# Performance work log

Hardware: AMD Instinct MI355X
Metric: run time of the kernel (lower is better)

The kernel has to match this reference:

```python
import jax, jax.numpy as jnp
import numpy as np

BATCH = 4096
NUM_CLASSES = 10000
FEAT_DIM = 512


def setup_inputs() -> dict:
    key = jax.random.key(0)
    k1, k2, k3 = jax.random.split(key, 3)
    x = jax.random.normal(k1, (BATCH, FEAT_DIM), dtype=jnp.float32)
    labels = jax.random.randint(k2, (BATCH,), 0, NUM_CLASSES)
    centers = jax.random.normal(k3, (NUM_CLASSES, FEAT_DIM), dtype=jnp.float32)
    lr = jnp.array([0.1], dtype=jnp.float32)
    return {"x": x, "labels": labels, "centers": centers, "lr": lr}


def reference(x, labels, centers, lr):
    batch, feat_dim = x.shape
    n_classes = centers.shape[0]

    # --- center update (vectorized replacement of the per-class/per-sample double loop) ---
    # A_j = count_j * centers[j] - sum_{i: label_i==j} x_i ;  delta_j = A_j / (1 + count_j)
    ones = jnp.ones((batch,), dtype=x.dtype)
    counts = jax.ops.segment_sum(ones, labels, num_segments=n_classes)          # [C]
    sum_x = jax.ops.segment_sum(x, labels, num_segments=n_classes)              # [C, D]
    delta = (counts[:, None] * centers - sum_x) / (1.0 + counts[:, None])       # [C, D]
    # torch wraps the result in a fresh nn.Parameter -> detached from autograd graph
    centers_new = jax.lax.stop_gradient(centers - lr[0] * delta)

    # --- pairwise squared distances, then 1/(1+d) ---
    d = (jnp.sum(x * x, axis=1, keepdims=True)                                   # [B, 1]
         + jnp.sum(centers_new * centers_new, axis=1)[None, :]                   # [1, C]
         - 2.0 * (x @ centers_new.T))                                            # [B, C]
    d = 1.0 / (1.0 + d)

    # --- masked reduction: row sum minus the own-class entry, clamped ---
    row_sum = d.sum(axis=1)                                                      # [B]
    own = jnp.take_along_axis(d, labels[:, None], axis=1)[:, 0]                  # [B]
    dist = jnp.clip(row_sum - own, 1e-12, 1e12)
    return dist.mean()
```

## Files before the change

kernel.cpp:

```cpp
#include <hip/hip_runtime.h>
#include <hip/hip_bf16.h>

#define BATCH 4096
#define NCLS  10000
#define CPAD  10240
#define FDIM  512
#define MAXL  32

typedef float f32x4 __attribute__((ext_vector_type(4)));
typedef int   ix4   __attribute__((ext_vector_type(4)));
typedef int   ix8   __attribute__((ext_vector_type(8)));

__device__ static inline void gld_lds16(const void* g, void* l) {
    __builtin_amdgcn_global_load_lds(
        (const __attribute__((address_space(1))) void*)g,
        (__attribute__((address_space(3))) void*)l, 16, 0, 0);
}

__device__ static inline unsigned int fp4e(float v) {
    unsigned int s = (__float_as_uint(v) >> 31) << 3;
    float a = fabsf(v);
    unsigned int c;
    if      (a < 1.25f) c = (a < 0.75f) ? (a < 0.25f ? 0u : 1u) : 2u;
    else if (a < 2.5f)  c = (a < 1.75f) ? 3u : 4u;
    else                c = (a < 3.5f) ? 5u : (a < 5.f ? 6u : 7u);
    return s | c;
}

__device__ static inline int pdst4(int row, int k) {
    return (row >> 4) * 4096 + (k >> 7) * 1024
         + ((k >> 5) & 3) * 256 + (row & 15) * 16 + ((k & 31) >> 1);
}

__global__ void prep_all(const float* __restrict__ x, const int* __restrict__ labels,
                         const float* __restrict__ centers, const float* __restrict__ lr,
                         unsigned char* __restrict__ xq, float* __restrict__ xnorm,
                         unsigned char* __restrict__ cq, float* __restrict__ cnorm,
                         float* __restrict__ out) {
    const int bid = blockIdx.x, t = threadIdx.x;
    __shared__ float red[4];
    if (bid < BATCH) {
        if (bid == 0 && t == 0) out[0] = 0.f;
        int i = bid;
        float2 v = *(const float2*)&x[(size_t)i * FDIM + 2 * t];
        xq[pdst4(i, 2 * t)] = (unsigned char)(fp4e(v.x) | (fp4e(v.y) << 4));
        float s = v.x * v.x + v.y * v.y;
#pragma unroll
        for (int m = 1; m < 64; m <<= 1) s += __shfl_xor(s, m);
        if ((t & 63) == 0) red[t >> 6] = s;
        __syncthreads();
        if (t == 0) xnorm[i] = red[0] + red[1] + red[2] + red[3];
        return;
    }
    int j = bid - BATCH;
    if (j >= NCLS) {
        cq[pdst4(j, 2 * t)] = 0;
        if (t == 0) cnorm[j] = 1e30f;
        return;
    }
    __shared__ int nmatch;
    __shared__ int idxs[MAXL];
    if (t == 0) nmatch = 0;
    __syncthreads();
    {
        const int4* l4 = (const int4*)labels;
        int4 a0 = l4[t], a1 = l4[t + 256], a2 = l4[t + 512], a3 = l4[t + 768];
#define CHK(V, B) { \
        if (V.x == j) { int p = atomicAdd(&nmatch, 1); if (p < MAXL) idxs[p] = (B); } \
        if (V.y == j) { int p = atomicAdd(&nmatch, 1); if (p < MAXL) idxs[p] = (B) + 1; } \
        if (V.z == j) { int p = atomicAdd(&nmatch, 1); if (p < MAXL) idxs[p] = (B) + 2; } \
        if (V.w == j) { int p = atomicAdd(&nmatch, 1); if (p < MAXL) idxs[p] = (B) + 3; } }
        CHK(a0, 4 * t) CHK(a1, 4 * (t + 256)) CHK(a2, 4 * (t + 512)) CHK(a3, 4 * (t + 768))
#undef CHK
    }
    __syncthreads();
    int cfull = nmatch;
    int c = cfull > MAXL ? MAXL : cfull;
    if (t == 0 && c > 1) {
        for (int a = 1; a < c; ++a) {
            int v = idxs[a]; int b = a - 1;
            while (b >= 0 && idxs[b] > v) { idxs[b + 1] = idxs[b]; --b; }
            idxs[b + 1] = v;
        }
    }
    __syncthreads();
    float cf  = (float)cfull;
    float lr0 = lr[0];
    float inv = 1.f / (1.f + cf);
    float c0 = centers[(size_t)j * FDIM + 2 * t];
    float c1 = centers[(size_t)j * FDIM + 2 * t + 1];
    float sx0 = 0.f, sx1 = 0.f;
    for (int q = 0; q < c; ++q) {
        const float* xr = &x[(size_t)idxs[q] * FDIM + 2 * t];
        sx0 += xr[0]; sx1 += xr[1];
    }
    float n0 = c0 - lr0 * (cf * c0 - sx0) * inv;
    float n1 = c1 - lr0 * (cf * c1 - sx1) * inv;
    cq[pdst4(j, 2 * t)] = (unsigned char)(fp4e(n0) | (fp4e(n1) << 4));
    float cn2 = n0 * n0 + n1 * n1;
#pragma unroll
    for (int m = 1; m < 64; m <<= 1) cn2 += __shfl_xor(cn2, m);
    if ((t & 63) == 0) red[t >> 6] = cn2;
    __syncthreads();
    if (t == 0) cnorm[j] = red[0] + red[1] + red[2] + red[3];
}

__global__ void __launch_bounds__(256, 2)
pairwise(const unsigned char* __restrict__ xq, const unsigned char* __restrict__ cq,
         const float* __restrict__ xnorm, const float* __restrict__ cnorm,
         const int* __restrict__ labels, float* __restrict__ row_part) {
    __shared__ unsigned char Als[32768];
    __shared__ unsigned char Bls[2][16384];
    __shared__ unsigned char Cnls[4096];
    const int tid = threadIdx.x;
    const int w = tid >> 6, lane = tid & 63;
    const int lr16 = lane & 15, lhi = lane >> 4;
    const int bid = blockIdx.x;
    const int swz = (bid & 7) * 64 + (bid >> 3);
    const int bx = swz & 31, g = swz >> 5;
    const int m_blk = bx * 128;
    const int mq = (w >> 1) * 64, nqh = (w & 1) * 32;

    float xn[4]; int lab[4];
#pragma unroll
    for (int mi = 0; mi < 4; ++mi) {
        int m_g = m_blk + mq + mi * 16 + lr16;
        xn[mi]  = xnorm[m_g];
        lab[mi] = labels[m_g];
    }
    {
        const unsigned char* gA = xq + (size_t)(m_blk >> 4) * 4096 + tid * 16;
#pragma unroll
        for (int q = 0; q < 8; ++q) gld_lds16(gA + q * 4096, &Als[q * 4096 + tid * 16]);
        gld_lds16((const char*)cnorm + (size_t)g * 2560 + tid * 16, &Cnls[tid * 16]);
        const unsigned char* gB0 = cq + (size_t)g * 40960 + tid * 16;
#pragma unroll
        for (int q = 0; q < 4; ++q) gld_lds16(gB0 + q * 4096, &Bls[0][q * 4096 + tid * 16]);
    }
    const unsigned char* gB = cq + (size_t)g * 40960 + tid * 16;

    ix8 afr[4][4];
    f32x4 acc[4][2];
    float rsum[4] = {0.f, 0.f, 0.f, 0.f};

    for (int s = 0; s < 10; ++s) {
        if (s < 9) {
            const unsigned char* gs = gB + (size_t)(s + 1) * 16384;
            unsigned char* ls = &Bls[(s + 1) & 1][0];
#pragma unroll
            for (int q = 0; q < 4; ++q) gld_lds16(gs + q * 4096, &ls[q * 4096 + tid * 16]);
            asm volatile("s_waitcnt vmcnt(4)" ::: "memory");
        } else {
            asm volatile("s_waitcnt vmcnt(0)" ::: "memory");
        }
        __builtin_amdgcn_s_barrier();

        if (s == 0) {
#pragma unroll
            for (int mi = 0; mi < 4; ++mi)
#pragma unroll
                for (int kt2 = 0; kt2 < 4; ++kt2) {
                    ix4 lo = *(const ix4*)&Als[((mq >> 4) + mi) * 4096 + kt2 * 1024 + lane * 16];
                    afr[mi][kt2] = __builtin_shufflevector(lo, lo, 0, 1, 2, 3, 0, 1, 2, 3);
                }
        }

#pragma unroll
        for (int mi = 0; mi < 4; ++mi)
#pragma unroll
            for (int ni = 0; ni < 2; ++ni) acc[mi][ni] = (f32x4)0.f;

        const unsigned char* bb = &Bls[s & 1][0];
#pragma unroll
        for (int kt2 = 0; kt2 < 4; ++kt2) {
            ix8 bg[2];
#pragma unroll
            for (int ni = 0; ni < 2; ++ni) {
                ix4 lo = *(const ix4*)&bb[((nqh >> 4) + ni) * 4096 + kt2 * 1024 + lane * 16];
                bg[ni] = __builtin_shufflevector(lo, lo, 0, 1, 2, 3, 0, 1, 2, 3);
            }
            __builtin_amdgcn_s_setprio(1);
#pragma unroll
            for (int mi = 0; mi < 4; ++mi)
#pragma unroll
                for (int ni = 0; ni < 2; ++ni)
                    acc[mi][ni] = __builtin_amdgcn_mfma_scale_f32_16x16x128_f8f6f4(
                        bg[ni], afr[mi][kt2], acc[mi][ni], 4, 4, 0, 0x7F7F7F7F, 0, 0x7F7F7F7F);
            __builtin_amdgcn_s_setprio(0);
        }
        __builtin_amdgcn_sched_barrier(0);
        __builtin_amdgcn_s_barrier();

        const float* cnf = (const float*)&Cnls[0];
        int nb_l = s * 64 + nqh;
        int nb_g = g * 640 + nb_l;
#pragma unroll
        for (int ni = 0; ni < 2; ++ni) {
#pragma unroll
            for (int r = 0; r < 4; ++r) {
                float cn = cnf[nb_l + ni * 16 + lhi * 4 + r];
                int n_g = nb_g + ni * 16 + lhi * 4 + r;
#pragma unroll
                for (int mi = 0; mi < 4; ++mi) {
                    float d1 = 1.f + xn[mi] + cn - 2.f * acc[mi][ni][r];
                    float rc = __builtin_amdgcn_rcpf(d1);
                    rsum[mi] += (n_g != lab[mi]) ? rc : 0.f;
                }
            }
        }
    }

#pragma unroll
    for (int mi = 0; mi < 4; ++mi) {
        rsum[mi] += __shfl_xor(rsum[mi], 16);
        rsum[mi] += __shfl_xor(rsum[mi], 32);
    }
    __syncthreads();
    float* spart = (float*)&Bls[0][0];
    if ((w & 1) && lhi == 0) {
#pragma unroll
        for (int mi = 0; mi < 4; ++mi)
            spart[mq + mi * 16 + lr16] = rsum[mi];
    }
    __syncthreads();
    if (!(w & 1) && lhi == 0) {
        float* rp = row_part + (size_t)g * BATCH + m_blk;
#pragma unroll
        for (int mi = 0; mi < 4; ++mi) {
            int ml = mq + mi * 16 + lr16;
            rp[ml] = rsum[mi] + spart[ml];
        }
    }
}

__global__ void finalize(const float* __restrict__ row_part, float* __restrict__ out) {
    int i = blockIdx.x * 256 + threadIdx.x;
    float s = 0.f;
#pragma unroll
    for (int p = 0; p < 16; ++p) s += row_part[(size_t)p * BATCH + i];
    float dist = fminf(fmaxf(s, 1e-12f), 1e12f);
    float v = dist * (1.f / BATCH);
#pragma unroll
    for (int m = 1; m < 64; m <<= 1) v += __shfl_xor(v, m);
    __shared__ float red[4];
    if ((threadIdx.x & 63) == 0) red[threadIdx.x >> 6] = v;
    __syncthreads();
    if (threadIdx.x == 0) atomicAdd(out, red[0] + red[1] + red[2] + red[3]);
}

extern "C" void kernel_launch(void* const* d_in, const int* in_sizes, int n_in,
                              void* d_out, int out_size, void* d_ws, size_t ws_size,
                              hipStream_t stream) {
    const float* x       = (const float*)d_in[0];
    const int*   labels  = (const int*)d_in[1];
    const float* centers = (const float*)d_in[2];
    const float* lr      = (const float*)d_in[3];
    float* out = (float*)d_out;

    char* ws = (char*)d_ws;
    size_t off = 0;
    unsigned char* cq = (unsigned char*)(ws + off); off += (size_t)CPAD * FDIM / 2;
    unsigned char* xq = (unsigned char*)(ws + off); off += (size_t)BATCH * FDIM / 2;
    float* cnorm    = (float*)(ws + off); off += (size_t)CPAD * 4;
    float* xnorm    = (float*)(ws + off); off += (size_t)BATCH * 4;
    float* row_part = (float*)(ws + off); off += (size_t)16 * BATCH * 4;

    prep_all<<<BATCH + CPAD, 256, 0, stream>>>(x, labels, centers, lr,
                                               xq, xnorm, cq, cnorm, out);
    pairwise<<<512, 256, 0, stream>>>(xq, cq, xnorm, cnorm, labels, row_part);
    finalize<<<BATCH / 256, 256, 0, stream>>>(row_part, out);
}
```

Measured before the change: 43.60 us.

## Build per-class sample lists with atomics, fuse finalize into pairwise kernel

A new small kernel buckets sample indices per class with global atomics. Each center-update block then reads its own short list instead of scanning all 4096 labels, which removes the redundant label traffic from roughly ten thousand blocks. The pairwise kernel now loads the A fragments straight into registers, dropping the 32KB A tile from LDS, and corrects the per-group B offset. The separate finalize kernel is replaced by a last-block-done counter inside pairwise. The cost is a memset plus an extra launch, and an atomic and fence at the end of every pairwise block.

Measured after the change: 79.54 us. 82.4% more time.

```diff
diff --git a/kernel.cpp b/kernel.cpp
--- a/kernel.cpp
+++ b/kernel.cpp
@@ -32,7 +32,16 @@
          + ((k >> 5) & 3) * 256 + (row & 15) * 16 + ((k & 31) >> 1);
 }
 
-__global__ void prep_all(const float* __restrict__ x, const int* __restrict__ labels,
+__global__ void build_lists(const int* __restrict__ labels, int* __restrict__ cnt,
+                            int* __restrict__ lists) {
+    int i = blockIdx.x * 256 + threadIdx.x;
+    int lab = labels[i];
+    int p = atomicAdd(&cnt[lab], 1);
+    if (p < MAXL) lists[lab * MAXL + p] = i;
+}
+
+__global__ void prep_all(const float* __restrict__ x, const int* __restrict__ cnt,
+                         const int* __restrict__ lists,
                          const float* __restrict__ centers, const float* __restrict__ lr,
                          unsigned char* __restrict__ xq, float* __restrict__ xnorm,
                          unsigned char* __restrict__ cq, float* __restrict__ cnorm,
@@ -58,24 +67,11 @@
         if (t == 0) cnorm[j] = 1e30f;
         return;
     }
-    __shared__ int nmatch;
+    int cfull = cnt[j];
+    int c = cfull > MAXL ? MAXL : cfull;
     __shared__ int idxs[MAXL];
-    if (t == 0) nmatch = 0;
-    __syncthreads();
-    {
-        const int4* l4 = (const int4*)labels;
-        int4 a0 = l4[t], a1 = l4[t + 256], a2 = l4[t + 512], a3 = l4[t + 768];
-#define CHK(V, B) { \
-        if (V.x == j) { int p = atomicAdd(&nmatch, 1); if (p < MAXL) idxs[p] = (B); } \
-        if (V.y == j) { int p = atomicAdd(&nmatch, 1); if (p < MAXL) idxs[p] = (B) + 1; } \
-        if (V.z == j) { int p = atomicAdd(&nmatch, 1); if (p < MAXL) idxs[p] = (B) + 2; } \
-        if (V.w == j) { int p = atomicAdd(&nmatch, 1); if (p < MAXL) idxs[p] = (B) + 3; } }
-        CHK(a0, 4 * t) CHK(a1, 4 * (t + 256)) CHK(a2, 4 * (t + 512)) CHK(a3, 4 * (t + 768))
-#undef CHK
-    }
-    __syncthreads();
-    int cfull = nmatch;
-    int c = cfull > MAXL ? MAXL : cfull;
+    if (t < c) idxs[t] = lists[j * MAXL + t];
+    __syncthreads();
     if (t == 0 && c > 1) {
         for (int a = 1; a < c; ++a) {
             int v = idxs[a]; int b = a - 1;
@@ -87,15 +83,14 @@
     float cf  = (float)cfull;
     float lr0 = lr[0];
     float inv = 1.f / (1.f + cf);
-    float c0 = centers[(size_t)j * FDIM + 2 * t];
-    float c1 = centers[(size_t)j * FDIM + 2 * t + 1];
+    float2 cv = *(const float2*)&centers[(size_t)j * FDIM + 2 * t];
     float sx0 = 0.f, sx1 = 0.f;
     for (int q = 0; q < c; ++q) {
-        const float* xr = &x[(size_t)idxs[q] * FDIM + 2 * t];
-        sx0 += xr[0]; sx1 += xr[1];
-    }
-    float n0 = c0 - lr0 * (cf * c0 - sx0) * inv;
-    float n1 = c1 - lr0 * (cf * c1 - sx1) * inv;
+        float2 xr = *(const float2*)&x[(size_t)idxs[q] * FDIM + 2 * t];
+        sx0 += xr.x; sx1 += xr.y;
+    }
+    float n0 = cv.x - lr0 * (cf * cv.x - sx0) * inv;
+    float n1 = cv.y - lr0 * (cf * cv.y - sx1) * inv;
     cq[pdst4(j, 2 * t)] = (unsigned char)(fp4e(n0) | (fp4e(n1) << 4));
     float cn2 = n0 * n0 + n1 * n1;
 #pragma unroll
@@ -108,8 +103,8 @@
 __global__ void __launch_bounds__(256, 2)
 pairwise(const unsigned char* __restrict__ xq, const unsigned char* __restrict__ cq,
          const float* __restrict__ xnorm, const float* __restrict__ cnorm,
-         const int* __restrict__ labels, float* __restrict__ row_part) {
-    __shared__ unsigned char Als[32768];
+         const int* __restrict__ labels, float* __restrict__ row_part,
+         int* __restrict__ done, float* __restrict__ out) {
     __shared__ unsigned char Bls[2][16384];
     __shared__ unsigned char Cnls[4096];
     const int tid = threadIdx.x;
@@ -128,18 +123,20 @@
         xn[mi]  = xnorm[m_g];
         lab[mi] = labels[m_g];
     }
-    {
-        const unsigned char* gA = xq + (size_t)(m_blk >> 4) * 4096 + tid * 16;
-#pragma unroll
-        for (int q = 0; q < 8; ++q) gld_lds16(gA + q * 4096, &Als[q * 4096 + tid * 16]);
-        gld_lds16((const char*)cnorm + (size_t)g * 2560 + tid * 16, &Cnls[tid * 16]);
-        const unsigned char* gB0 = cq + (size_t)g * 40960 + tid * 16;
-#pragma unroll
-        for (int q = 0; q < 4; ++q) gld_lds16(gB0 + q * 4096, &Bls[0][q * 4096 + tid * 16]);
-    }
-    const unsigned char* gB = cq + (size_t)g * 40960 + tid * 16;
-
     ix8 afr[4][4];
+#pragma unroll
+    for (int mi = 0; mi < 4; ++mi)
+#pragma unroll
+        for (int kt2 = 0; kt2 < 4; ++kt2) {
+            ix4 lo = *(const ix4*)(xq + (size_t)((m_blk >> 4) + (mq >> 4) + mi) * 4096
+                                      + kt2 * 1024 + lane * 16);
+            afr[mi][kt2] = __builtin_shufflevector(lo, lo, 0, 1, 2, 3, 0, 1, 2, 3);
+        }
+    gld_lds16((const char*)cnorm + (size_t)g * 2560 + tid * 16, &Cnls[tid * 16]);
+    const unsigned char* gB = cq + (size_t)g * 163840 + tid * 16;
+#pragma unroll
+    for (int q = 0; q < 4; ++q) gld_lds16(gB + q * 4096, &Bls[0][q * 4096 + tid * 16]);
+
     f32x4 acc[4][2];
     float rsum[4] = {0.f, 0.f, 0.f, 0.f};
 
@@ -154,16 +151,6 @@
             asm volatile("s_waitcnt vmcnt(0)" ::: "memory");
         }
         __builtin_amdgcn_s_barrier();
-
-        if (s == 0) {
-#pragma unroll
-            for (int mi = 0; mi < 4; ++mi)
-#pragma unroll
-                for (int kt2 = 0; kt2 < 4; ++kt2) {
-                    ix4 lo = *(const ix4*)&Als[((mq >> 4) + mi) * 4096 + kt2 * 1024 + lane * 16];
-                    afr[mi][kt2] = __builtin_shufflevector(lo, lo, 0, 1, 2, 3, 0, 1, 2, 3);
-                }
-        }
 
 #pragma unroll
         for (int mi = 0; mi < 4; ++mi)
@@ -231,21 +218,29 @@
             rp[ml] = rsum[mi] + spart[ml];
         }
     }
-}
-
-__global__ void finalize(const float* __restrict__ row_part, float* __restrict__ out) {
-    int i = blockIdx.x * 256 + threadIdx.x;
-    float s = 0.f;
-#pragma unroll
-    for (int p = 0; p < 16; ++p) s += row_part[(size_t)p * BATCH + i];
-    float dist = fminf(fmaxf(s, 1e-12f), 1e12f);
-    float v = dist * (1.f / BATCH);
-#pragma unroll
-    for (int m = 1; m < 64; m <<= 1) v += __shfl_xor(v, m);
-    __shared__ float red[4];
-    if ((threadIdx.x & 63) == 0) red[threadIdx.x >> 6] = v;
-    __syncthreads();
-    if (threadIdx.x == 0) atomicAdd(out, red[0] + red[1] + red[2] + red[3]);
+
+    __threadfence();
+    __shared__ int amlast;
+    if (tid == 0) amlast = (atomicAdd(&done[bx], 1) == 15) ? 1 : 0;
+    __syncthreads();
+    if (amlast) {
+        __threadfence();
+        float v = 0.f;
+        if (tid < 128) {
+            int i = m_blk + tid;
+            float ssum = 0.f;
+#pragma unroll
+            for (int p = 0; p < 16; ++p) ssum += row_part[(size_t)p * BATCH + i];
+            float dist = fminf(fmaxf(ssum, 1e-12f), 1e12f);
+            v = dist * (1.f / BATCH);
+#pragma unroll
+            for (int m = 1; m < 64; m <<= 1) v += __shfl_xor(v, m);
+        }
+        __shared__ float red2[2];
+        if (tid < 128 && lane == 0) red2[w] = v;
+        __syncthreads();
+        if (tid == 0) atomicAdd(out, red2[0] + red2[1]);
+    }
 }
 
 extern "C" void kernel_launch(void* const* d_in, const int* in_sizes, int n_in,
@@ -264,9 +259,13 @@
     float* cnorm    = (float*)(ws + off); off += (size_t)CPAD * 4;
     float* xnorm    = (float*)(ws + off); off += (size_t)BATCH * 4;
     float* row_part = (float*)(ws + off); off += (size_t)16 * BATCH * 4;
-
-    prep_all<<<BATCH + CPAD, 256, 0, stream>>>(x, labels, centers, lr,
+    int*   cnt      = (int*)(ws + off);   off += (size_t)NCLS * 4;
+    int*   done     = (int*)(ws + off);   off += 32 * 4;
+    int*   lists    = (int*)(ws + off);   off += (size_t)NCLS * MAXL * 4;
+
+    hipMemsetAsync(cnt, 0, (size_t)NCLS * 4 + 32 * 4, stream);
+    build_lists<<<BATCH / 256, 256, 0, stream>>>(labels, cnt, lists);
+    prep_all<<<BATCH + CPAD, 256, 0, stream>>>(x, cnt, lists, centers, lr,
                                                xq, xnorm, cq, cnorm, out);
-    pairwise<<<512, 256, 0, stream>>>(xq, cq, xnorm, cnorm, labels, row_part);
-    finalize<<<BATCH / 256, 256, 0, stream>>>(row_part, out);
-}
+    pairwise<<<512, 256, 0, stream>>>(xq, cq, xnorm, cnorm, labels, row_part, done, out);
+}
```
